# Kernel optimization log

Measured on AMD Instinct MI355X. Metric: run time of the kernel, lower is better.

Reference implementation:

```python
import jax, jax.numpy as jnp
import numpy as np

HEADS = 16
HEAD_DIM = 64
EMB = 1024
B, S = 4, 2048
SCALE = 1.0 / 8.0  # fixed constant in the original code
MASK_PENALTY = -50.0  # original adds -50 * upper_triangular, not -inf


def setup_inputs() -> dict:
    key = jax.random.key(0)
    ks = jax.random.split(key, 5)
    x = jax.random.normal(ks[0], (B, S, EMB), dtype=jnp.float32)
    Wq = jax.random.normal(ks[1], (EMB, HEADS * HEAD_DIM), dtype=jnp.float32) * 0.02
    Wk = jax.random.normal(ks[2], (EMB, HEADS * HEAD_DIM), dtype=jnp.float32) * 0.02
    Wv = jax.random.normal(ks[3], (EMB, HEADS * HEAD_DIM), dtype=jnp.float32) * 0.02
    Wr = jax.random.normal(ks[4], (HEADS * HEAD_DIM, EMB), dtype=jnp.float32) * 0.02
    return {"x": x, "Wq": Wq, "Wk": Wk, "Wv": Wv, "Wr": Wr}


def reference(x, Wq, Wk, Wv, Wr):
    b, s, _ = x.shape
    # project and split heads: [b, s, h, d]
    q = (x @ Wq).reshape(b, s, HEADS, HEAD_DIM)
    k = (x @ Wk).reshape(b, s, HEADS, HEAD_DIM)
    v = (x @ Wv).reshape(b, s, HEADS, HEAD_DIM)
    # scores: [b, h, s, s]
    scores = SCALE * jnp.einsum('bqhd,bkhd->bhqk', q, k)
    # causal additive mask: -50 on strictly-upper triangle (faithful to original)
    causal = jnp.triu(jnp.ones((s, s), dtype=x.dtype), k=1)
    scores = scores + MASK_PENALTY * causal
    attn = jax.nn.softmax(scores, axis=-1)
    out = jnp.einsum('bhqk,bkhd->bqhd', attn, v).reshape(b, s, HEADS * HEAD_DIM)
    return out @ Wr
```

## Files before the change

### kernel.cpp

```cpp
#include <hip/hip_runtime.h>

typedef _Float16 f16;
typedef _Float16 f16x8 __attribute__((ext_vector_type(8)));
typedef _Float16 f16x4 __attribute__((ext_vector_type(4)));
typedef float f32x4 __attribute__((ext_vector_type(4)));

#define MFMA16(A, B, C) __builtin_amdgcn_mfma_f32_16x16x32_f16((A), (B), (C), 0, 0, 0)

__device__ __forceinline__ void async16(void* lds, const void* gp) {
    __builtin_amdgcn_global_load_lds(
        (__attribute__((address_space(1))) void*)(gp),
        (__attribute__((address_space(3))) void*)(lds), 16, 0, 0);
}

__global__ __launch_bounds__(256) void k_convert(const float* __restrict__ in,
                                                 f16* __restrict__ out, int n) {
    int i = (blockIdx.x * 256 + threadIdx.x) * 4;
    if (i + 3 < n) {
        float4 v = *(const float4*)(in + i);
        f16x4 o = {(f16)v.x, (f16)v.y, (f16)v.z, (f16)v.w};
        *(f16x4*)(out + i) = o;
    }
}

__global__ __launch_bounds__(256) void k_transpose_w4(const float* __restrict__ Wq,
                                                      const float* __restrict__ Wk,
                                                      const float* __restrict__ Wv,
                                                      const float* __restrict__ Wr,
                                                      f16* __restrict__ Wqkvt,
                                                      f16* __restrict__ Wrt) {
    __shared__ float tile[32][33];
    int z = blockIdx.z;
    const float* W = (z == 0) ? Wq : (z == 1) ? Wk : (z == 2) ? Wv : Wr;
    f16* Wt = (z == 3) ? Wrt : Wqkvt + z * 1048576;
    int c0 = blockIdx.x * 32, r0 = blockIdx.y * 32;
    int tx = threadIdx.x, ty = threadIdx.y;
#pragma unroll
    for (int j = 0; j < 32; j += 8)
        tile[ty + j][tx] = W[(r0 + ty + j) * 1024 + c0 + tx];
    __syncthreads();
#pragma unroll
    for (int j = 0; j < 32; j += 8)
        Wt[(c0 + ty + j) * 1024 + r0 + tx] = (f16)tile[tx][ty + j];
}

__global__ __launch_bounds__(256) void k_transpose_v(const f16* __restrict__ QKV,
                                                     f16* __restrict__ Vt) {
    __shared__ f16 tile[32][33];
    int s0 = blockIdx.x * 32;
    int d0 = blockIdx.y * 32;
    int bh = blockIdx.z;
    int b = bh >> 4, h = bh & 15;
    int tx = threadIdx.x, ty = threadIdx.y;
#pragma unroll
    for (int j = 0; j < 32; j += 8)
        tile[ty + j][tx] = QKV[(b * 2048 + s0 + ty + j) * 3072 + 2048 + h * 64 + d0 + tx];
    __syncthreads();
#pragma unroll
    for (int j = 0; j < 32; j += 8)
        Vt[(bh * 64 + d0 + ty + j) * 2048 + s0 + tx] = tile[tx][ty + j];
}

template <bool OUT_F16>
__global__ __launch_bounds__(256) void k_gemm_bt(const f16* __restrict__ A,
                                                 const f16* __restrict__ Bt,
                                                 void* __restrict__ Cv,
                                                 int M, int N, int K) {
    __shared__ f16 As[128][32];
    __shared__ f16 Bs[128][32];
    int t = threadIdx.x;
    int lane = t & 63, w = t >> 6;
    int wm = (w >> 1) * 64, wn = (w & 1) * 64;
    int m0 = blockIdx.y * 128, n0 = blockIdx.x * 128;
    int ln = lane & 15, g = lane >> 4;

    int lin0 = w * 128 + lane, lin1 = lin0 + 64;
    int r0 = lin0 >> 2, c0 = (lin0 & 3) ^ ((r0 >> 1) & 3);
    int r1 = lin1 >> 2, c1 = (lin1 & 3) ^ ((r1 >> 1) & 3);
    const f16* gA0 = A + (size_t)(m0 + r0) * K + c0 * 8;
    const f16* gA1 = A + (size_t)(m0 + r1) * K + c1 * 8;
    const f16* gB0 = Bt + (size_t)(n0 + r0) * K + c0 * 8;
    const f16* gB1 = Bt + (size_t)(n0 + r1) * K + c1 * 8;
    f16* lA0 = &As[0][0] + w * 1024;
    f16* lB0 = &Bs[0][0] + w * 1024;

    f32x4 acc[4][4] = {};
    int sw = (ln >> 1) & 3;

    for (int k0 = 0; k0 < K; k0 += 32) {
        __syncthreads();
        async16(lA0, gA0 + k0);
        async16(lA0 + 512, gA1 + k0);
        async16(lB0, gB0 + k0);
        async16(lB0 + 512, gB1 + k0);
        __syncthreads();
        f16x8 af[4], bf[4];
#pragma unroll
        for (int i = 0; i < 4; i++) {
            af[i] = *(const f16x8*)&As[wm + i * 16 + ln][(g ^ sw) * 8];
            bf[i] = *(const f16x8*)&Bs[wn + i * 16 + ln][(g ^ sw) * 8];
        }
#pragma unroll
        for (int mt = 0; mt < 4; mt++)
#pragma unroll
            for (int nt = 0; nt < 4; nt++)
                acc[mt][nt] = MFMA16(af[mt], bf[nt], acc[mt][nt]);
    }

    int rg = g * 4;
#pragma unroll
    for (int mt = 0; mt < 4; mt++)
#pragma unroll
        for (int nt = 0; nt < 4; nt++)
#pragma unroll
            for (int r = 0; r < 4; r++) {
                int row = m0 + wm + mt * 16 + rg + r;
                int col = n0 + wn + nt * 16 + ln;
                float v = acc[mt][nt][r];
                if (OUT_F16)
                    ((f16*)Cv)[(size_t)row * N + col] = (f16)v;
                else
                    ((float*)Cv)[(size_t)row * N + col] = v;
            }
}

__global__ __launch_bounds__(256, 2) void k_attn(const f16* __restrict__ QKV,
                                                 const f16* __restrict__ Vt,
                                                 f16* __restrict__ Ob) {
    __shared__ f16 Ks[64][72];
    __shared__ f16 Vs[64][72];
    __shared__ f16 Ps[128][72];
    int pi = blockIdx.x, bh = blockIdx.y;
    int b = bh >> 4, h = bh & 15;
    int t = threadIdx.x, lane = t & 63, wq = t >> 6;
    int ln = lane & 15, g = lane >> 4, g8 = g * 8, rg = g * 4;

    int c0 = t, c1 = t + 256;
    int kr0 = c0 >> 3, kc0 = (c0 & 7) * 8;
    int kr1 = c1 >> 3, kc1 = (c1 & 7) * 8;
    const f16* Kbase = QKV + (size_t)b * 2048 * 3072 + 1024 + h * 64;
    const f16* Vbase = Vt + (size_t)bh * 64 * 2048;

    const float C_SCL = 0.18033688f;
    const float C_MSK = -72.134752f;
    f16x8 ones;
#pragma unroll
    for (int j = 0; j < 8; j++) ones[j] = (f16)1.f;

    int4 rk0 = *(const int4*)(Kbase + (size_t)kr0 * 3072 + kc0);
    int4 rk1 = *(const int4*)(Kbase + (size_t)kr1 * 3072 + kc1);
    int4 rv0 = *(const int4*)(Vbase + (size_t)kr0 * 2048 + kc0);
    int4 rv1 = *(const int4*)(Vbase + (size_t)kr1 * 2048 + kc1);

    for (int phase = 0; phase < 2; phase++) {
        int qt = (phase == 0) ? (15 - pi) : pi;
        int q0 = qt * 128;
        int nk = q0 / 64 + 2;

        f16x8 bq[2][2];
#pragma unroll
        for (int nt = 0; nt < 2; nt++)
#pragma unroll
            for (int kd = 0; kd < 2; kd++)
                bq[nt][kd] = *(const f16x8*)(QKV +
                    (size_t)(b * 2048 + q0 + wq * 32 + nt * 16 + ln) * 3072 +
                    h * 64 + kd * 32 + g8);

        f32x4 oacc[2][4] = {};
        f32x4 osum[2] = {};

        for (int kt = 0; kt < nk; kt++) {
            int k0 = kt * 64;
            __syncthreads();
            *(int4*)&Ks[kr0][kc0] = rk0;
            *(int4*)&Ks[kr1][kc1] = rk1;
            *(int4*)&Vs[kr0][kc0] = rv0;
            *(int4*)&Vs[kr1][kc1] = rv1;
            if (kt + 1 < nk) {
                int kn = k0 + 64;
                rk0 = *(const int4*)(Kbase + (size_t)(kn + kr0) * 3072 + kc0);
                rk1 = *(const int4*)(Kbase + (size_t)(kn + kr1) * 3072 + kc1);
                rv0 = *(const int4*)(Vbase + (size_t)kr0 * 2048 + kn + kc0);
                rv1 = *(const int4*)(Vbase + (size_t)kr1 * 2048 + kn + kc1);
            } else if (phase == 0) {
                rk0 = *(const int4*)(Kbase + (size_t)kr0 * 3072 + kc0);
                rk1 = *(const int4*)(Kbase + (size_t)kr1 * 3072 + kc1);
                rv0 = *(const int4*)(Vbase + (size_t)kr0 * 2048 + kc0);
                rv1 = *(const int4*)(Vbase + (size_t)kr1 * 2048 + kc1);
            }
            __syncthreads();

            if (k0 > q0 + wq * 32 + 31) continue;

            f32x4 sacc[4][2] = {};
#pragma unroll
            for (int kd = 0; kd < 2; kd++) {
                f16x8 ak[4];
#pragma unroll
                for (int mt = 0; mt < 4; mt++)
                    ak[mt] = *(const f16x8*)&Ks[mt * 16 + ln][kd * 32 + g8];
#pragma unroll
                for (int mt = 0; mt < 4; mt++)
#pragma unroll
                    for (int nt = 0; nt < 2; nt++)
                        sacc[mt][nt] = MFMA16(ak[mt], bq[nt][kd], sacc[mt][nt]);
            }

            bool needs_mask = (k0 + 63 > q0 + wq * 32);
#pragma unroll
            for (int nt = 0; nt < 2; nt++) {
                int q = q0 + wq * 32 + nt * 16 + ln;
#pragma unroll
                for (int mt = 0; mt < 4; mt++) {
                    f16x4 pk;
#pragma unroll
                    for (int r = 0; r < 4; r++) {
                        float e;
                        if (needs_mask) {
                            int kk = k0 + mt * 16 + rg + r;
                            e = __builtin_amdgcn_exp2f(
                                fmaf(sacc[mt][nt][r], C_SCL, (kk > q) ? C_MSK : 0.f));
                        } else {
                            e = __builtin_amdgcn_exp2f(sacc[mt][nt][r] * C_SCL);
                        }
                        pk[r] = (f16)e;
                    }
                    *(f16x4*)&Ps[wq * 32 + nt * 16 + ln][mt * 16 + rg] = pk;
                }
            }

#pragma unroll
            for (int kk = 0; kk < 2; kk++) {
                f16x8 ap[2], bv[4];
#pragma unroll
                for (int mt = 0; mt < 2; mt++)
                    ap[mt] = *(const f16x8*)&Ps[wq * 32 + mt * 16 + ln][kk * 32 + g8];
#pragma unroll
                for (int dt = 0; dt < 4; dt++)
                    bv[dt] = *(const f16x8*)&Vs[dt * 16 + ln][kk * 32 + g8];
#pragma unroll
                for (int mt = 0; mt < 2; mt++) {
#pragma unroll
                    for (int dt = 0; dt < 4; dt++)
                        oacc[mt][dt] = MFMA16(ap[mt], bv[dt], oacc[mt][dt]);
                    osum[mt] = MFMA16(ap[mt], ones, osum[mt]);
                }
            }
        }

#pragma unroll
        for (int mt = 0; mt < 2; mt++)
#pragma unroll
            for (int r = 0; r < 4; r++) {
                float inv = __builtin_amdgcn_rcpf(osum[mt][r]);
                int row = b * 2048 + q0 + wq * 32 + mt * 16 + rg + r;
#pragma unroll
                for (int dt = 0; dt < 4; dt++)
                    Ob[(size_t)row * 1024 + h * 64 + dt * 16 + ln] =
                        (f16)(oacc[mt][dt][r] * inv);
            }
    }
}

extern "C" void kernel_launch(void* const* d_in, const int* in_sizes, int n_in,
                              void* d_out, int out_size, void* d_ws, size_t ws_size,
                              hipStream_t stream) {
    const float* x = (const float*)d_in[0];
    const float* Wq = (const float*)d_in[1];
    const float* Wk = (const float*)d_in[2];
    const float* Wv = (const float*)d_in[3];
    const float* Wr = (const float*)d_in[4];
    float* out = (float*)d_out;

    f16* ws = (f16*)d_ws;
    f16* xb    = ws;
    f16* Wqkvt = xb + 8388608;
    f16* Wrt   = Wqkvt + 3145728;
    f16* QKVb  = Wrt + 1048576;
    f16* Vtb   = QKVb + 25165824;
    f16* Obuf  = Vtb + 8388608;

    k_convert<<<8192, 256, 0, stream>>>(x, xb, 8388608);
    dim3 tb(32, 8);
    k_transpose_w4<<<dim3(32, 32, 4), tb, 0, stream>>>(Wq, Wk, Wv, Wr, Wqkvt, Wrt);
    k_gemm_bt<true><<<dim3(24, 64), 256, 0, stream>>>(xb, Wqkvt, QKVb, 8192, 3072, 1024);
    k_transpose_v<<<dim3(64, 2, 64), tb, 0, stream>>>(QKVb, Vtb);
    k_attn<<<dim3(8, 64), 256, 0, stream>>>(QKVb, Vtb, Obuf);
    k_gemm_bt<false><<<dim3(8, 64), 256, 0, stream>>>(Obuf, Wrt, out, 8192, 1024, 1024);
}
```

Baseline: 285.2 us.

## Use 32x32 MFMA in GEMM and split attention into one block per query tile

The GEMM switches from 16x16x32 MFMA tiles to 32x32x16 MFMA with 2x2 accumulators per wave and raises launch bounds to 4 blocks per CU. The attention kernel stops pairing a long and short query tile per block and launches one block per (batch-head, query tile), ordered heaviest-first, with occupancy hint raised to 4. The aim is fewer LDS fragment loads per MFMA in the GEMMs and more parallelism and occupancy in attention. The risks are register pressure from the launch bounds and load imbalance now left to the hardware scheduler.

```diff
diff --git a/kernel.cpp b/kernel.cpp
--- a/kernel.cpp
+++ b/kernel.cpp
@@ -4,8 +4,10 @@
 typedef _Float16 f16x8 __attribute__((ext_vector_type(8)));
 typedef _Float16 f16x4 __attribute__((ext_vector_type(4)));
 typedef float f32x4 __attribute__((ext_vector_type(4)));
+typedef float f32x16 __attribute__((ext_vector_type(16)));
 
 #define MFMA16(A, B, C) __builtin_amdgcn_mfma_f32_16x16x32_f16((A), (B), (C), 0, 0, 0)
+#define MFMA32(A, B, C) __builtin_amdgcn_mfma_f32_32x32x16_f16((A), (B), (C), 0, 0, 0)
 
 __device__ __forceinline__ void async16(void* lds, const void* gp) {
     __builtin_amdgcn_global_load_lds(
@@ -62,17 +64,18 @@
 }
 
 template <bool OUT_F16>
-__global__ __launch_bounds__(256) void k_gemm_bt(const f16* __restrict__ A,
-                                                 const f16* __restrict__ Bt,
-                                                 void* __restrict__ Cv,
-                                                 int M, int N, int K) {
+__global__ __launch_bounds__(256, 4) void k_gemm_bt(const f16* __restrict__ A,
+                                                    const f16* __restrict__ Bt,
+                                                    void* __restrict__ Cv,
+                                                    int M, int N, int K) {
     __shared__ f16 As[128][32];
     __shared__ f16 Bs[128][32];
     int t = threadIdx.x;
     int lane = t & 63, w = t >> 6;
     int wm = (w >> 1) * 64, wn = (w & 1) * 64;
     int m0 = blockIdx.y * 128, n0 = blockIdx.x * 128;
-    int ln = lane & 15, g = lane >> 4;
+    int ln = lane & 31, kh = lane >> 5;
+    int sw = (ln >> 1) & 3;
 
     int lin0 = w * 128 + lane, lin1 = lin0 + 64;
     int r0 = lin0 >> 2, c0 = (lin0 & 3) ^ ((r0 >> 1) & 3);
@@ -84,8 +87,7 @@
     f16* lA0 = &As[0][0] + w * 1024;
     f16* lB0 = &Bs[0][0] + w * 1024;
 
-    f32x4 acc[4][4] = {};
-    int sw = (ln >> 1) & 3;
+    f32x16 acc[2][2] = {};
 
     for (int k0 = 0; k0 < K; k0 += 32) {
         __syncthreads();
@@ -94,28 +96,32 @@
         async16(lB0, gB0 + k0);
         async16(lB0 + 512, gB1 + k0);
         __syncthreads();
-        f16x8 af[4], bf[4];
-#pragma unroll
-        for (int i = 0; i < 4; i++) {
-            af[i] = *(const f16x8*)&As[wm + i * 16 + ln][(g ^ sw) * 8];
-            bf[i] = *(const f16x8*)&Bs[wn + i * 16 + ln][(g ^ sw) * 8];
-        }
-#pragma unroll
-        for (int mt = 0; mt < 4; mt++)
-#pragma unroll
-            for (int nt = 0; nt < 4; nt++)
-                acc[mt][nt] = MFMA16(af[mt], bf[nt], acc[mt][nt]);
+#pragma unroll
+        for (int kd = 0; kd < 2; kd++) {
+            int c = kd * 2 + kh;
+            f16x8 af[2], bf[2];
+#pragma unroll
+            for (int mt = 0; mt < 2; mt++)
+                af[mt] = *(const f16x8*)&As[wm + mt * 32 + ln][(c ^ sw) * 8];
+#pragma unroll
+            for (int nt = 0; nt < 2; nt++)
+                bf[nt] = *(const f16x8*)&Bs[wn + nt * 32 + ln][(c ^ sw) * 8];
+#pragma unroll
+            for (int mt = 0; mt < 2; mt++)
+#pragma unroll
+                for (int nt = 0; nt < 2; nt++)
+                    acc[mt][nt] = MFMA32(af[mt], bf[nt], acc[mt][nt]);
+        }
     }
 
-    int rg = g * 4;
-#pragma unroll
-    for (int mt = 0; mt < 4; mt++)
-#pragma unroll
-        for (int nt = 0; nt < 4; nt++)
-#pragma unroll
-            for (int r = 0; r < 4; r++) {
-                int row = m0 + wm + mt * 16 + rg + r;
-                int col = n0 + wn + nt * 16 + ln;
+#pragma unroll
+    for (int mt = 0; mt < 2; mt++)
+#pragma unroll
+        for (int nt = 0; nt < 2; nt++)
+#pragma unroll
+            for (int r = 0; r < 16; r++) {
+                int row = m0 + wm + mt * 32 + (r & 3) + 8 * (r >> 2) + 4 * kh;
+                int col = n0 + wn + nt * 32 + ln;
                 float v = acc[mt][nt][r];
                 if (OUT_F16)
                     ((f16*)Cv)[(size_t)row * N + col] = (f16)v;
@@ -124,14 +130,16 @@
             }
 }
 
-__global__ __launch_bounds__(256, 2) void k_attn(const f16* __restrict__ QKV,
+__global__ __launch_bounds__(256, 4) void k_attn(const f16* __restrict__ QKV,
                                                  const f16* __restrict__ Vt,
                                                  f16* __restrict__ Ob) {
     __shared__ f16 Ks[64][72];
     __shared__ f16 Vs[64][72];
     __shared__ f16 Ps[128][72];
-    int pi = blockIdx.x, bh = blockIdx.y;
+    int bh = blockIdx.x;
+    int qt = 15 - (int)blockIdx.y;
     int b = bh >> 4, h = bh & 15;
+    int q0 = qt * 128;
     int t = threadIdx.x, lane = t & 63, wq = t >> 6;
     int ln = lane & 15, g = lane >> 4, g8 = g * 8, rg = g * 4;
 
@@ -147,119 +155,109 @@
 #pragma unroll
     for (int j = 0; j < 8; j++) ones[j] = (f16)1.f;
 
+    f16x8 bq[2][2];
+#pragma unroll
+    for (int nt = 0; nt < 2; nt++)
+#pragma unroll
+        for (int kd = 0; kd < 2; kd++)
+            bq[nt][kd] = *(const f16x8*)(QKV +
+                (size_t)(b * 2048 + q0 + wq * 32 + nt * 16 + ln) * 3072 +
+                h * 64 + kd * 32 + g8);
+
     int4 rk0 = *(const int4*)(Kbase + (size_t)kr0 * 3072 + kc0);
     int4 rk1 = *(const int4*)(Kbase + (size_t)kr1 * 3072 + kc1);
     int4 rv0 = *(const int4*)(Vbase + (size_t)kr0 * 2048 + kc0);
     int4 rv1 = *(const int4*)(Vbase + (size_t)kr1 * 2048 + kc1);
 
-    for (int phase = 0; phase < 2; phase++) {
-        int qt = (phase == 0) ? (15 - pi) : pi;
-        int q0 = qt * 128;
-        int nk = q0 / 64 + 2;
-
-        f16x8 bq[2][2];
-#pragma unroll
-        for (int nt = 0; nt < 2; nt++)
-#pragma unroll
-            for (int kd = 0; kd < 2; kd++)
-                bq[nt][kd] = *(const f16x8*)(QKV +
-                    (size_t)(b * 2048 + q0 + wq * 32 + nt * 16 + ln) * 3072 +
-                    h * 64 + kd * 32 + g8);
-
-        f32x4 oacc[2][4] = {};
-        f32x4 osum[2] = {};
-
-        for (int kt = 0; kt < nk; kt++) {
-            int k0 = kt * 64;
-            __syncthreads();
-            *(int4*)&Ks[kr0][kc0] = rk0;
-            *(int4*)&Ks[kr1][kc1] = rk1;
-            *(int4*)&Vs[kr0][kc0] = rv0;
-            *(int4*)&Vs[kr1][kc1] = rv1;
-            if (kt + 1 < nk) {
-                int kn = k0 + 64;
-                rk0 = *(const int4*)(Kbase + (size_t)(kn + kr0) * 3072 + kc0);
-                rk1 = *(const int4*)(Kbase + (size_t)(kn + kr1) * 3072 + kc1);
-                rv0 = *(const int4*)(Vbase + (size_t)kr0 * 2048 + kn + kc0);
-                rv1 = *(const int4*)(Vbase + (size_t)kr1 * 2048 + kn + kc1);
-            } else if (phase == 0) {
-                rk0 = *(const int4*)(Kbase + (size_t)kr0 * 3072 + kc0);
-                rk1 = *(const int4*)(Kbase + (size_t)kr1 * 3072 + kc1);
-                rv0 = *(const int4*)(Vbase + (size_t)kr0 * 2048 + kc0);
-                rv1 = *(const int4*)(Vbase + (size_t)kr1 * 2048 + kc1);
+    f32x4 oacc[2][4] = {};
+    f32x4 osum[2] = {};
+    int nk = q0 / 64 + 2;
+
+    for (int kt = 0; kt < nk; kt++) {
+        int k0 = kt * 64;
+        __syncthreads();
+        *(int4*)&Ks[kr0][kc0] = rk0;
+        *(int4*)&Ks[kr1][kc1] = rk1;
+        *(int4*)&Vs[kr0][kc0] = rv0;
+        *(int4*)&Vs[kr1][kc1] = rv1;
+        if (kt + 1 < nk) {
+            int kn = k0 + 64;
+            rk0 = *(const int4*)(Kbase + (size_t)(kn + kr0) * 3072 + kc0);
+            rk1 = *(const int4*)(Kbase + (size_t)(kn + kr1) * 3072 + kc1);
+            rv0 = *(const int4*)(Vbase + (size_t)kr0 * 2048 + kn + kc0);
+            rv1 = *(const int4*)(Vbase + (size_t)kr1 * 2048 + kn + kc1);
+        }
+        __syncthreads();
+
+        if (k0 > q0 + wq * 32 + 31) continue;
+
+        f32x4 sacc[4][2] = {};
+#pragma unroll
+        for (int kd = 0; kd < 2; kd++) {
+            f16x8 ak[4];
+#pragma unroll
+            for (int mt = 0; mt < 4; mt++)
+                ak[mt] = *(const f16x8*)&Ks[mt * 16 + ln][kd * 32 + g8];
+#pragma unroll
+            for (int mt = 0; mt < 4; mt++)
+#pragma unroll
+                for (int nt = 0; nt < 2; nt++)
+                    sacc[mt][nt] = MFMA16(ak[mt], bq[nt][kd], sacc[mt][nt]);
+        }
+
+        bool needs_mask = (k0 + 63 > q0 + wq * 32);
+#pragma unroll
+        for (int nt = 0; nt < 2; nt++) {
+            int q = q0 + wq * 32 + nt * 16 + ln;
+#pragma unroll
+            for (int mt = 0; mt < 4; mt++) {
+                f16x4 pk;
+#pragma unroll
+                for (int r = 0; r < 4; r++) {
+                    float e;
+                    if (needs_mask) {
+                        int kk = k0 + mt * 16 + rg + r;
+                        e = __builtin_amdgcn_exp2f(
+                            fmaf(sacc[mt][nt][r], C_SCL, (kk > q) ? C_MSK : 0.f));
+                    } else {
+                        e = __builtin_amdgcn_exp2f(sacc[mt][nt][r] * C_SCL);
+                    }
+                    pk[r] = (f16)e;
+                }
+                *(f16x4*)&Ps[wq * 32 + nt * 16 + ln][mt * 16 + rg] = pk;
             }
-            __syncthreads();
-
-            if (k0 > q0 + wq * 32 + 31) continue;
-
-            f32x4 sacc[4][2] = {};
-#pragma unroll
-            for (int kd = 0; kd < 2; kd++) {
-                f16x8 ak[4];
-#pragma unroll
-                for (int mt = 0; mt < 4; mt++)
-                    ak[mt] = *(const f16x8*)&Ks[mt * 16 + ln][kd * 32 + g8];
-#pragma unroll
-                for (int mt = 0; mt < 4; mt++)
-#pragma unroll
-                    for (int nt = 0; nt < 2; nt++)
-                        sacc[mt][nt] = MFMA16(ak[mt], bq[nt][kd], sacc[mt][nt]);
+        }
+
+#pragma unroll
+        for (int kk = 0; kk < 2; kk++) {
+            f16x8 ap[2], bv[4];
+#pragma unroll
+            for (int mt = 0; mt < 2; mt++)
+                ap[mt] = *(const f16x8*)&Ps[wq * 32 + mt * 16 + ln][kk * 32 + g8];
+#pragma unroll
+            for (int dt = 0; dt < 4; dt++)
+                bv[dt] = *(const f16x8*)&Vs[dt * 16 + ln][kk * 32 + g8];
+#pragma unroll
+            for (int mt = 0; mt < 2; mt++) {
+#pragma unroll
+                for (int dt = 0; dt < 4; dt++)
+                    oacc[mt][dt] = MFMA16(ap[mt], bv[dt], oacc[mt][dt]);
+                osum[mt] = MFMA16(ap[mt], ones, osum[mt]);
             }
-
-            bool needs_mask = (k0 + 63 > q0 + wq * 32);
-#pragma unroll
-            for (int nt = 0; nt < 2; nt++) {
-                int q = q0 + wq * 32 + nt * 16 + ln;
-#pragma unroll
-                for (int mt = 0; mt < 4; mt++) {
-                    f16x4 pk;
-#pragma unroll
-                    for (int r = 0; r < 4; r++) {
-                        float e;
-                        if (needs_mask) {
-                            int kk = k0 + mt * 16 + rg + r;
-                            e = __builtin_amdgcn_exp2f(
-                                fmaf(sacc[mt][nt][r], C_SCL, (kk > q) ? C_MSK : 0.f));
-                        } else {
-                            e = __builtin_amdgcn_exp2f(sacc[mt][nt][r] * C_SCL);
-                        }
-                        pk[r] = (f16)e;
-                    }
-                    *(f16x4*)&Ps[wq * 32 + nt * 16 + ln][mt * 16 + rg] = pk;
-                }
-            }
-
-#pragma unroll
-            for (int kk = 0; kk < 2; kk++) {
-                f16x8 ap[2], bv[4];
-#pragma unroll
-                for (int mt = 0; mt < 2; mt++)
-                    ap[mt] = *(const f16x8*)&Ps[wq * 32 + mt * 16 + ln][kk * 32 + g8];
-#pragma unroll
-                for (int dt = 0; dt < 4; dt++)
-                    bv[dt] = *(const f16x8*)&Vs[dt * 16 + ln][kk * 32 + g8];
-#pragma unroll
-                for (int mt = 0; mt < 2; mt++) {
-#pragma unroll
-                    for (int dt = 0; dt < 4; dt++)
-                        oacc[mt][dt] = MFMA16(ap[mt], bv[dt], oacc[mt][dt]);
-                    osum[mt] = MFMA16(ap[mt], ones, osum[mt]);
-                }
-            }
-        }
-
-#pragma unroll
-        for (int mt = 0; mt < 2; mt++)
-#pragma unroll
-            for (int r = 0; r < 4; r++) {
-                float inv = __builtin_amdgcn_rcpf(osum[mt][r]);
-                int row = b * 2048 + q0 + wq * 32 + mt * 16 + rg + r;
-#pragma unroll
-                for (int dt = 0; dt < 4; dt++)
-                    Ob[(size_t)row * 1024 + h * 64 + dt * 16 + ln] =
-                        (f16)(oacc[mt][dt][r] * inv);
-            }
+        }
     }
+
+#pragma unroll
+    for (int mt = 0; mt < 2; mt++)
+#pragma unroll
+        for (int r = 0; r < 4; r++) {
+            float inv = __builtin_amdgcn_rcpf(osum[mt][r]);
+            int row = b * 2048 + q0 + wq * 32 + mt * 16 + rg + r;
+#pragma unroll
+            for (int dt = 0; dt < 4; dt++)
+                Ob[(size_t)row * 1024 + h * 64 + dt * 16 + ln] =
+                    (f16)(oacc[mt][dt][r] * inv);
+        }
 }
 
 extern "C" void kernel_launch(void* const* d_in, const int* in_sizes, int n_in,
@@ -285,6 +283,6 @@
     k_transpose_w4<<<dim3(32, 32, 4), tb, 0, stream>>>(Wq, Wk, Wv, Wr, Wqkvt, Wrt);
     k_gemm_bt<true><<<dim3(24, 64), 256, 0, stream>>>(xb, Wqkvt, QKVb, 8192, 3072, 1024);
     k_transpose_v<<<dim3(64, 2, 64), tb, 0, stream>>>(QKVb, Vtb);
-    k_attn<<<dim3(8, 64), 256, 0, stream>>>(QKVb, Vtb, Obuf);
+    k_attn<<<dim3(64, 16), 256, 0, stream>>>(QKVb, Vtb, Obuf);
     k_gemm_bt<false><<<dim3(8, 64), 256, 0, stream>>>(Obuf, Wrt, out, 8192, 1024, 1024);
 }
```

New measurement: 294.5 us. 1.03x slower.
